# Optimization experiments

Measured on AMD Instinct MI355X. Metric: run time of the kernel, lower is better.

## Reference

```python
import jax, jax.numpy as jnp
import numpy as np

NUM_HEADS = 8
HEAD_DIM = 64
D_MODEL = NUM_HEADS * HEAD_DIM  # 512
B, T = 4, 2048


def setup_inputs() -> dict:
    key = jax.random.key(0)
    k1, k2 = jax.random.split(key)
    x = jax.random.normal(k1, (B, T, D_MODEL), dtype=jnp.float32)
    mask = jnp.ones((B, 1, T, T), dtype=jnp.float32)
    W = jax.random.normal(k2, (D_MODEL, 3 * D_MODEL), dtype=jnp.float32) * (D_MODEL ** -0.5)
    b = jnp.zeros((3 * D_MODEL,), dtype=jnp.float32)
    return {"x": x, "mask": mask, "W": W, "b": b}


def reference(x, mask, W, b):
    batch = x.shape[0]
    # fused QKV projection: [B, T, 3D]
    qkv = jnp.einsum("btd,de->bte", x, W) + b
    # NOTE: faithful to torch reshape [B, T, H, Hd, 3] -> the size-3 axis is innermost
    qkv = qkv.reshape(batch, -1, NUM_HEADS, HEAD_DIM, 3)
    qkv = jnp.transpose(qkv, (4, 0, 2, 1, 3))  # [3, B, H, T, Hd]
    q, k, v = qkv[0], qkv[1], qkv[2]
    logits = jnp.einsum("bhqd,bhkd->bhqk", q, k) / (HEAD_DIM ** 0.5)
    logits = logits + (1.0 - mask) * -10000.0
    w = jax.nn.softmax(logits, axis=-1)
    out = jnp.einsum("bhqk,bhkd->bhqd", w, v)  # [B, H, T, Hd]
    out = jnp.transpose(out, (0, 2, 1, 3)).reshape(batch, -1, NUM_HEADS * HEAD_DIM)
    return out
```

## Files before the change

kernel.cpp:

```cpp
#include <hip/hip_runtime.h>
#include <hip/hip_bf16.h>
#include <stdint.h>

#define B_   4
#define T_   2048
#define H_   8
#define HD_  64
#define DM_  512
#define N3_  1536

typedef short bf_el;
typedef __attribute__((ext_vector_type(8))) bf_el bfrag;
typedef __attribute__((ext_vector_type(4))) bf_el bhalf4;
typedef __attribute__((ext_vector_type(4))) float ffrag;

#define SCALE_L2E  0.18033688011112043f
#define MASK_L2E   14426.950408889634f

static __device__ __forceinline__ unsigned short f2bf(float f) {
    union { float f; unsigned int i; } v; v.f = f;
    unsigned int r = v.i + 0x7fff + ((v.i >> 16) & 1);
    return (unsigned short)(r >> 16);
}
static __device__ __forceinline__ unsigned short f2bf_fast(float f) {
    union { float f; unsigned int i; } v; v.f = f;
    return (unsigned short)((v.i + 0x8000u) >> 16);
}

static __device__ __forceinline__ unsigned int cvt_pk_bf16(float a, float b) {
    unsigned int r;
    asm("v_cvt_pk_bf16_f32 %0, %1, %2" : "=v"(r) : "v"(a), "v"(b));
    return r;
}

typedef __attribute__((address_space(1))) const unsigned int gu32;
typedef __attribute__((address_space(3))) unsigned int lu32;
static __device__ __forceinline__ void glds16(const unsigned short* g, unsigned short* l) {
    __builtin_amdgcn_global_load_lds((gu32*)g, (lu32*)l, 16, 0, 0);
}

#define VMCNT(n) do { asm volatile("s_waitcnt vmcnt(" #n ")" ::: "memory"); \
                      __builtin_amdgcn_sched_barrier(0); } while (0)

__global__ __launch_bounds__(256) void k_prep(const float* __restrict__ W,
                                              const float* __restrict__ X,
                                              const float* __restrict__ mask,
                                              unsigned short* __restrict__ Wt,
                                              unsigned short* __restrict__ Xb,
                                              int* __restrict__ flags) {
    __shared__ __align__(16) unsigned short Ls[64 * 72];
    const int bid = blockIdx.x;
    const int tid = threadIdx.x;

    if (bid < 512) {
        const int R0 = bid * 16;
        const int mb = R0 >> 11;
        const int q0 = R0 & 2047;
        const int e  = mb * 32 + (q0 >> 6);
        const int wave = tid >> 6, lane = tid & 63;
        unsigned int acc = 0u;
        const float* base = mask + (size_t)R0 * T_ + tid * 8;
#pragma unroll
        for (int rr = 0; rr < 16; ++rr) {
            const uint4 u0 = *(const uint4*)(base + (size_t)rr * T_);
            const uint4 u1 = *(const uint4*)(base + (size_t)rr * T_ + 4);
            acc |= (u0.x ^ 0x3F800000u) | (u0.y ^ 0x3F800000u) |
                   (u0.z ^ 0x3F800000u) | (u0.w ^ 0x3F800000u) |
                   (u1.x ^ 0x3F800000u) | (u1.y ^ 0x3F800000u) |
                   (u1.z ^ 0x3F800000u) | (u1.w ^ 0x3F800000u);
        }
        unsigned long long bal = __ballot(acc != 0u);
        if (lane == 0 && bal != 0ULL) {
            unsigned int bits = 0u;
#pragma unroll
            for (int j = 0; j < 8; ++j)
                if ((bal >> (8 * j)) & 0xFFULL)
                    bits |= (1u << (wave * 8 + j));
            atomicOr((unsigned int*)&flags[e], bits);
        }
        return;
    }
    if (bid < 768) {
        const int b2 = bid - 512;
        const float* src = X + (size_t)b2 * 16384;
        unsigned short* dst = Xb + (size_t)b2 * 16384;
#pragma unroll
        for (int j = 0; j < 8; ++j) {
            int idx = j * 512 + tid * 2;
            float4 f0 = *(const float4*)(src + idx * 4);
            float4 f1 = *(const float4*)(src + idx * 4 + 4);
            __align__(16) unsigned short t8[8];
            t8[0] = f2bf_fast(f0.x); t8[1] = f2bf_fast(f0.y);
            t8[2] = f2bf_fast(f0.z); t8[3] = f2bf_fast(f0.w);
            t8[4] = f2bf_fast(f1.x); t8[5] = f2bf_fast(f1.y);
            t8[6] = f2bf_fast(f1.z); t8[7] = f2bf_fast(f1.w);
            *(uint4*)(dst + idx * 4) = *(const uint4*)t8;
        }
        return;
    }
    {
        const int t  = bid - 768;
        const int n0 = (t % 24) * 64;
        const int k0 = (t / 24) * 64;
#pragma unroll
        for (int i = 0; i < 4; ++i) {
            int chunk = tid + i * 256;
            int k = chunk >> 4;
            int c = chunk & 15;
            float4 f = *(const float4*)(W + (size_t)(k0 + k) * N3_ + n0 + c * 4);
            unsigned short* p = Ls + k * 72 + c * 4;
            p[0] = f2bf(f.x); p[1] = f2bf(f.y); p[2] = f2bf(f.z); p[3] = f2bf(f.w);
        }
        __syncthreads();
        const int n = tid >> 2;
        const int g = tid & 3;
        __align__(16) unsigned short tmp[16];
#pragma unroll
        for (int i = 0; i < 16; ++i) tmp[i] = Ls[(g * 16 + i) * 72 + n];
        uint4* dst = (uint4*)(Wt + (size_t)(n0 + n) * DM_ + k0 + g * 16);
        dst[0] = *(const uint4*)(tmp);
        dst[1] = *(const uint4*)(tmp + 8);
    }
}

__global__ __launch_bounds__(256) void k_gemm_qkv(const unsigned short* __restrict__ Xb,
                                                  const unsigned short* __restrict__ Wt,
                                                  const float* __restrict__ bias,
                                                  unsigned short* __restrict__ Qb,
                                                  unsigned short* __restrict__ Kb,
                                                  unsigned short* __restrict__ Vtb) {
    __shared__ __align__(16) unsigned short SH[12800];
    unsigned short* As = SH;
    unsigned short* Bs = SH + 5120;
    unsigned short* Cs = SH;

    const int tid  = threadIdx.x;
    const int wave = tid >> 6;
    const int lane = tid & 63;
    const int quad = lane >> 4;
    const int l16  = lane & 15;
    const int wm = wave >> 1, wn = wave & 1;
    const int h  = blockIdx.x >> 6;
    const int m0 = (blockIdx.x & 63) * 128;
    const int n0 = h * 192;

    float bvv[6];
#pragma unroll
    for (int ni = 0; ni < 6; ++ni) bvv[ni] = bias[n0 + wn * 96 + ni * 16 + l16];

    ffrag acc[4][6];
#pragma unroll
    for (int i = 0; i < 4; ++i)
#pragma unroll
        for (int j = 0; j < 6; ++j) acc[i][j] = (ffrag){0.f, 0.f, 0.f, 0.f};

    for (int kt = 0; kt < 16; ++kt) {
        __syncthreads();
#pragma unroll
        for (int i = 0; i < 2; ++i) {
            int chunk = tid + i * 256;
            int r = chunk >> 2, c = chunk & 3;
            *(uint4*)(As + r * 40 + c * 8) =
                *(const uint4*)(Xb + (size_t)(m0 + r) * DM_ + kt * 32 + c * 8);
        }
#pragma unroll
        for (int i = 0; i < 3; ++i) {
            int chunk = tid + i * 256;
            int r = chunk >> 2, c = chunk & 3;
            *(uint4*)(Bs + r * 40 + c * 8) =
                *(const uint4*)(Wt + (size_t)(n0 + r) * DM_ + kt * 32 + c * 8);
        }
        __syncthreads();
        bfrag af[4], bfr[6];
#pragma unroll
        for (int mi = 0; mi < 4; ++mi)
            af[mi] = *(const bfrag*)(As + (wm * 64 + mi * 16 + l16) * 40 + quad * 8);
#pragma unroll
        for (int ni = 0; ni < 6; ++ni)
            bfr[ni] = *(const bfrag*)(Bs + (wn * 96 + ni * 16 + l16) * 40 + quad * 8);
#pragma unroll
        for (int mi = 0; mi < 4; ++mi)
#pragma unroll
            for (int ni = 0; ni < 6; ++ni)
                acc[mi][ni] = __builtin_amdgcn_mfma_f32_16x16x32_bf16(af[mi], bfr[ni], acc[mi][ni], 0, 0, 0);
    }

    const int b   = m0 >> 11;
    const int tb0 = m0 & 2047;
    const size_t bh = (size_t)(b * 8 + h);
    float cscale[6];
#pragma unroll
    for (int ni = 0; ni < 6; ++ni) {
        int c = wn * 96 + ni * 16 + l16;
        cscale[ni] = (c % 3 == 0) ? SCALE_L2E : 1.0f;
    }
#pragma unroll
    for (int half = 0; half < 2; ++half) {
        __syncthreads();
        if (wm == half) {
#pragma unroll
            for (int mi = 0; mi < 4; ++mi)
#pragma unroll
                for (int ni = 0; ni < 6; ++ni)
#pragma unroll
                    for (int reg = 0; reg < 4; ++reg) {
                        int r = mi * 16 + quad * 4 + reg;
                        int c = wn * 96 + ni * 16 + l16;
                        Cs[r * 200 + c] = f2bf_fast((acc[mi][ni][reg] + bvv[ni]) * cscale[ni]);
                    }
        }
        __syncthreads();
        const int tb = tb0 + half * 64;
#pragma unroll
        for (int i = 0; i < 2; ++i) {
            int idx = tid + i * 256;
            int tl = idx >> 3, hc = (idx & 7) * 8;
            __align__(16) unsigned short tq[8], tk[8];
#pragma unroll
            for (int j = 0; j < 8; ++j) {
                tq[j] = Cs[tl * 200 + (hc + j) * 3 + 0];
                tk[j] = Cs[tl * 200 + (hc + j) * 3 + 1];
            }
            *(uint4*)(Qb + (bh * T_ + tb + tl) * HD_ + hc) = *(const uint4*)tq;
            *(uint4*)(Kb + (bh * T_ + tb + tl) * HD_ + hc) = *(const uint4*)tk;
        }
#pragma unroll
        for (int i = 0; i < 2; ++i) {
            int idx = tid + i * 256;
            int hd = idx >> 3, t8 = (idx & 7) * 8;
            __align__(16) unsigned short tv[8];
#pragma unroll
            for (int j = 0; j < 8; ++j)
                tv[j] = Cs[(t8 + j) * 200 + hd * 3 + 2];
            *(uint4*)(Vtb + (bh * HD_ + hd) * T_ + tb + t8) = *(const uint4*)tv;
        }
    }
}

__global__ __launch_bounds__(256, 2) void k_attn(const unsigned short* __restrict__ Q,
                                                 const unsigned short* __restrict__ K,
                                                 const unsigned short* __restrict__ Vt,
                                                 const float* __restrict__ mask,
                                                 const int* __restrict__ flags,
                                                 float* __restrict__ out) {
    __shared__ __align__(16) unsigned short SH[32768];
    __shared__ float Rs[256];

    const int tid = threadIdx.x;
    const int wave = tid >> 6, lane = tid & 63;
    const int quad = lane >> 4, l16 = lane & 15;
    const int rg = wave & 1;
    const int kh = wave >> 1;
    const int bh = blockIdx.x & 31, b = bh >> 3, h = bh & 7;
    const int qt = blockIdx.x >> 5;
    const int q0 = qt * 128;

    bfrag qf[4][2];
#pragma unroll
    for (int g = 0; g < 4; ++g) {
        size_t qrow = ((size_t)bh * T_ + q0 + rg * 64 + g * 16 + l16) * HD_;
        qf[g][0] = *(const bfrag*)(Q + qrow + quad * 8);
        qf[g][1] = *(const bfrag*)(Q + qrow + 32 + quad * 8);
    }
    ffrag of[4][5];
#pragma unroll
    for (int g = 0; g < 4; ++g)
#pragma unroll
        for (int nb = 0; nb < 5; ++nb) of[g][nb] = (ffrag){0.f, 0.f, 0.f, 0.f};

    bfrag vones;
#pragma unroll
    for (int j = 0; j < 8; ++j) vones[j] = (short)0x3F80;

    const unsigned int flbits = ((const unsigned int*)flags)[b * 32 + qt * 2 + rg];

    const int lrow = lane >> 3, lcol = lane & 7, swz = lcol ^ lrow;
    const int voffK = lrow * 64 + swz * 8;
    const size_t voffV = (size_t)(wave * 16 + lrow) * T_ + swz * 8;
    const unsigned short* Kbh = K  + (size_t)bh * T_ * HD_;
    const unsigned short* Vbh = Vt + (size_t)bh * HD_ * T_;

    auto STAGE = [&](int buf, int kt) {
        unsigned short* KL = &SH[buf * 4096] + wave * 1024;
        unsigned short* VL = &SH[16384 + buf * 4096] + wave * 1024;
        const unsigned short* kg = Kbh + (size_t)kt * 4096 + wave * 1024 + voffK;
        const unsigned short* vg = Vbh + (size_t)kt * 64 + voffV;
        glds16(kg, KL);
        glds16(kg + 512, KL + 512);
        glds16(vg, VL);
        glds16(vg + (size_t)8 * T_, VL + 512);
    };

    STAGE(0, 0);
    STAGE(1, 1);

    for (int kt = 0; kt < 32; ++kt) {
        if (kt < 30) STAGE((kt + 2) & 3, kt + 2);
        if (kt < 30)      { VMCNT(8); }
        else if (kt == 30){ VMCNT(4); }
        else              { VMCNT(0); }
        __builtin_amdgcn_s_barrier();

        const int cur = kt & 3;
        const unsigned short* KLc = &SH[cur * 4096];
        const unsigned short* VLc = &SH[16384 + cur * 4096];

        bfrag kf[2][2];
#pragma unroll
        for (int ns = 0; ns < 2; ++ns) {
            const int r = (kh * 2 + ns) * 16 + l16;
#pragma unroll
            for (int ks = 0; ks < 2; ++ks)
                kf[ns][ks] = *(const bfrag*)(KLc + r * 64 + (((ks * 4 + quad) ^ (l16 & 7)) * 8));
        }
        bhalf4 vf[2][4];
#pragma unroll
        for (int nb = 0; nb < 4; ++nb) {
            const int d = nb * 16 + l16;
#pragma unroll
            for (int ns = 0; ns < 2; ++ns)
                vf[ns][nb] = *(const bhalf4*)(VLc + d * 64 +
                                ((kh * 32 + ns * 16 + quad * 4) ^ ((l16 & 7) * 8)));
        }

        const int fl = (int)((flbits >> kt) & 1u);
#pragma unroll
        for (int g = 0; g < 4; ++g) {
            ffrag st[2];
            __builtin_amdgcn_s_setprio(1);
#pragma unroll
            for (int ns = 0; ns < 2; ++ns) {
                ffrag a = (ffrag){0.f, 0.f, 0.f, 0.f};
                a = __builtin_amdgcn_mfma_f32_16x16x32_bf16(kf[ns][0], qf[g][0], a, 0, 0, 0);
                a = __builtin_amdgcn_mfma_f32_16x16x32_bf16(kf[ns][1], qf[g][1], a, 0, 0, 0);
                st[ns] = a;
            }
            __builtin_amdgcn_s_setprio(0);
            float p[2][4];
            if (fl) {
                const float* mrow = mask + ((size_t)b * T_ + q0 + rg * 64 + g * 16 + l16) * T_
                                  + kt * 64 + kh * 32 + quad * 4;
#pragma unroll
                for (int ns = 0; ns < 2; ++ns) {
                    float mv[4];
                    *(float4*)mv = *(const float4*)(mrow + ns * 16);
#pragma unroll
                    for (int reg = 0; reg < 4; ++reg)
                        p[ns][reg] = __builtin_amdgcn_exp2f(
                            fmaf(mv[reg], MASK_L2E, st[ns][reg] - MASK_L2E));
                }
            } else {
#pragma unroll
                for (int ns = 0; ns < 2; ++ns)
#pragma unroll
                    for (int reg = 0; reg < 4; ++reg)
                        p[ns][reg] = __builtin_amdgcn_exp2f(st[ns][reg]);
            }
            union { unsigned int u[4]; bfrag s; } pa;
            pa.u[0] = cvt_pk_bf16(p[0][0], p[0][1]);
            pa.u[1] = cvt_pk_bf16(p[0][2], p[0][3]);
            pa.u[2] = cvt_pk_bf16(p[1][0], p[1][1]);
            pa.u[3] = cvt_pk_bf16(p[1][2], p[1][3]);
            __builtin_amdgcn_s_setprio(1);
#pragma unroll
            for (int nb = 0; nb < 4; ++nb) {
                union { bhalf4 h[2]; bfrag f; } vv;
                vv.h[0] = vf[0][nb];
                vv.h[1] = vf[1][nb];
                of[g][nb] = __builtin_amdgcn_mfma_f32_16x16x32_bf16(pa.s, vv.f, of[g][nb], 0, 0, 0);
            }
            of[g][4] = __builtin_amdgcn_mfma_f32_16x16x32_bf16(pa.s, vones, of[g][4], 0, 0, 0);
            __builtin_amdgcn_s_setprio(0);
        }
    }

    __syncthreads();
    float* Fp = (float*)SH;
    if (l16 == 0) {
#pragma unroll
        for (int g = 0; g < 4; ++g)
#pragma unroll
            for (int reg = 0; reg < 4; ++reg)
                Rs[kh * 128 + rg * 64 + g * 16 + quad * 4 + reg] = of[g][4][reg];
    }
    if (kh == 1) {
        float* basep = Fp + rg * (64 * 66);
#pragma unroll
        for (int g = 0; g < 4; ++g)
#pragma unroll
            for (int nb = 0; nb < 4; ++nb)
#pragma unroll
                for (int reg = 0; reg < 4; ++reg)
                    basep[(g * 16 + quad * 4 + reg) * 66 + nb * 16 + l16] = of[g][nb][reg];
    }
    __syncthreads();
    if (kh == 0) {
        const float* basep = Fp + rg * (64 * 66);
#pragma unroll
        for (int g = 0; g < 4; ++g) {
            float inv[4];
#pragma unroll
            for (int reg = 0; reg < 4; ++reg) {
                int row = rg * 64 + g * 16 + quad * 4 + reg;
                inv[reg] = 1.0f / (Rs[row] + Rs[128 + row]);
            }
#pragma unroll
            for (int nb = 0; nb < 4; ++nb)
#pragma unroll
                for (int reg = 0; reg < 4; ++reg) {
                    float v = of[g][nb][reg] + basep[(g * 16 + quad * 4 + reg) * 66 + nb * 16 + l16];
                    int t = q0 + rg * 64 + g * 16 + quad * 4 + reg;
                    out[((size_t)b * T_ + t) * DM_ + h * 64 + nb * 16 + l16] = v * inv[reg];
                }
        }
    }
}

extern "C" void kernel_launch(void* const* d_in, const int* in_sizes, int n_in,
                              void* d_out, int out_size, void* d_ws, size_t ws_size,
                              hipStream_t stream) {
    const float* X    = (const float*)d_in[0];
    const float* mask = (const float*)d_in[1];
    const float* W    = (const float*)d_in[2];
    const float* bias = (const float*)d_in[3];
    float* outp = (float*)d_out;

    char* ws = (char*)d_ws;
    unsigned short* Wt  = (unsigned short*)(ws);
    unsigned short* Xb  = (unsigned short*)(ws + 1572864);
    unsigned short* Qb  = (unsigned short*)(ws + 9961472);
    unsigned short* Kb  = (unsigned short*)(ws + 18350080);
    unsigned short* Vtb = (unsigned short*)(ws + 26738688);
    int*            flg = (int*)(ws + 35127296);

    hipMemsetAsync(flg, 0, 512, stream);
    k_prep     <<<dim3(960), 256, 0, stream>>>(W, X, mask, Wt, Xb, flg);
    k_gemm_qkv <<<dim3(512), 256, 0, stream>>>(Xb, Wt, bias, Qb, Kb, Vtb);
    k_attn     <<<dim3(512), 256, 0, stream>>>(Qb, Kb, Vtb, mask, flg, outp);
}
```

Before: 196.3 us.

## Double-buffer QKV GEMM tiles and replace flag memset/atomics with per-block byte writes

The QKV GEMM now prefetches the next K-slice into registers while MFMAs run on the current shared-memory buffer, then writes it to a second LDS buffer. This leaves one barrier per iteration instead of two and overlaps global loads with compute. The mask-flag scan now has each wave store a byte into a dedicated slot instead of doing an atomicOr, so the hipMemsetAsync before the kernels can be dropped. The attention kernel ORs four words to rebuild the flags. Doubling LDS may reduce occupancy, and the flag buffer now grows to 2KB, which must fit inside the workspace.

```diff
diff --git a/kernel.cpp b/kernel.cpp
--- a/kernel.cpp
+++ b/kernel.cpp
@@ -70,13 +70,13 @@
                    (u1.z ^ 0x3F800000u) | (u1.w ^ 0x3F800000u);
         }
         unsigned long long bal = __ballot(acc != 0u);
-        if (lane == 0 && bal != 0ULL) {
-            unsigned int bits = 0u;
+        if (lane == 0) {
+            unsigned int byte = 0u;
 #pragma unroll
             for (int j = 0; j < 8; ++j)
-                if ((bal >> (8 * j)) & 0xFFULL)
-                    bits |= (1u << (wave * 8 + j));
-            atomicOr((unsigned int*)&flags[e], bits);
+                if ((bal >> (8 * j)) & 0xFFULL) byte |= (1u << j);
+            ((unsigned char*)flags)[((size_t)e * 4 + (bid & 3)) * 4 + wave] =
+                (unsigned char)byte;
         }
         return;
     }
@@ -129,9 +129,7 @@
                                                   unsigned short* __restrict__ Qb,
                                                   unsigned short* __restrict__ Kb,
                                                   unsigned short* __restrict__ Vtb) {
-    __shared__ __align__(16) unsigned short SH[12800];
-    unsigned short* As = SH;
-    unsigned short* Bs = SH + 5120;
+    __shared__ __align__(16) unsigned short SH[25600];
     unsigned short* Cs = SH;
 
     const int tid  = threadIdx.x;
@@ -154,23 +152,46 @@
 #pragma unroll
         for (int j = 0; j < 6; ++j) acc[i][j] = (ffrag){0.f, 0.f, 0.f, 0.f};
 
-    for (int kt = 0; kt < 16; ++kt) {
-        __syncthreads();
+    uint4 areg[2], breg[3];
+    auto GLOAD = [&](int kt) {
 #pragma unroll
         for (int i = 0; i < 2; ++i) {
             int chunk = tid + i * 256;
             int r = chunk >> 2, c = chunk & 3;
-            *(uint4*)(As + r * 40 + c * 8) =
-                *(const uint4*)(Xb + (size_t)(m0 + r) * DM_ + kt * 32 + c * 8);
+            areg[i] = *(const uint4*)(Xb + (size_t)(m0 + r) * DM_ + kt * 32 + c * 8);
         }
 #pragma unroll
         for (int i = 0; i < 3; ++i) {
             int chunk = tid + i * 256;
             int r = chunk >> 2, c = chunk & 3;
-            *(uint4*)(Bs + r * 40 + c * 8) =
-                *(const uint4*)(Wt + (size_t)(n0 + r) * DM_ + kt * 32 + c * 8);
-        }
-        __syncthreads();
+            breg[i] = *(const uint4*)(Wt + (size_t)(n0 + r) * DM_ + kt * 32 + c * 8);
+        }
+    };
+    auto SWRITE = [&](int buf) {
+        unsigned short* As = SH + buf * 12800;
+        unsigned short* Bs = As + 5120;
+#pragma unroll
+        for (int i = 0; i < 2; ++i) {
+            int chunk = tid + i * 256;
+            int r = chunk >> 2, c = chunk & 3;
+            *(uint4*)(As + r * 40 + c * 8) = areg[i];
+        }
+#pragma unroll
+        for (int i = 0; i < 3; ++i) {
+            int chunk = tid + i * 256;
+            int r = chunk >> 2, c = chunk & 3;
+            *(uint4*)(Bs + r * 40 + c * 8) = breg[i];
+        }
+    };
+
+    GLOAD(0); SWRITE(0);
+    __syncthreads();
+
+    for (int kt = 0; kt < 16; ++kt) {
+        const int cur = kt & 1;
+        if (kt < 15) GLOAD(kt + 1);
+        const unsigned short* As = SH + cur * 12800;
+        const unsigned short* Bs = As + 5120;
         bfrag af[4], bfr[6];
 #pragma unroll
         for (int mi = 0; mi < 4; ++mi)
@@ -183,6 +204,10 @@
 #pragma unroll
             for (int ni = 0; ni < 6; ++ni)
                 acc[mi][ni] = __builtin_amdgcn_mfma_f32_16x16x32_bf16(af[mi], bfr[ni], acc[mi][ni], 0, 0, 0);
+        if (kt < 15) {
+            SWRITE(cur ^ 1);
+            __syncthreads();
+        }
     }
 
     const int b   = m0 >> 11;
@@ -272,7 +297,9 @@
 #pragma unroll
     for (int j = 0; j < 8; ++j) vones[j] = (short)0x3F80;
 
-    const unsigned int flbits = ((const unsigned int*)flags)[b * 32 + qt * 2 + rg];
+    const int e = b * 32 + qt * 2 + rg;
+    const int4 fw = *(const int4*)(flags + (size_t)e * 4);
+    const unsigned int flbits = (unsigned int)(fw.x | fw.y | fw.z | fw.w);
 
     const int lrow = lane >> 3, lcol = lane & 7, swz = lcol ^ lrow;
     const int voffK = lrow * 64 + swz * 8;
@@ -433,7 +460,6 @@
     unsigned short* Vtb = (unsigned short*)(ws + 26738688);
     int*            flg = (int*)(ws + 35127296);
 
-    hipMemsetAsync(flg, 0, 512, stream);
     k_prep     <<<dim3(960), 256, 0, stream>>>(W, X, mask, Wt, Xb, flg);
     k_gemm_qkv <<<dim3(512), 256, 0, stream>>>(Xb, Wt, bias, Qb, Kb, Vtb);
     k_attn     <<<dim3(512), 256, 0, stream>>>(Qb, Kb, Vtb, mask, flg, outp);
```

New measurement: 221.3 us. 12.7% more time.

## Pipeline QKV GEMM loads via async global-to-LDS and drop flag memset

Applied to the files above, without the earlier changes.

The QKV GEMM now stages A and B tiles straight into LDS with async global-to-LDS loads, using a 4-deep ring buffer with two tiles in flight. Progress is tracked with vmcnt waits and a single barrier, and the LDS layout is XOR-swizzled, which removes the register round-trip and one of the two syncthreads per k-step. The mask-flag pass now writes a plain byte per wave into an expanded flag array that attention ORs back together, so the memset launch and the atomics go away. The cost is much more LDS per block (80 KB), which may limit occupancy. The flag buffer grows 4x, so the workspace layout must still fit.

```diff
diff --git a/kernel.cpp b/kernel.cpp
--- a/kernel.cpp
+++ b/kernel.cpp
@@ -70,13 +70,13 @@
                    (u1.z ^ 0x3F800000u) | (u1.w ^ 0x3F800000u);
         }
         unsigned long long bal = __ballot(acc != 0u);
-        if (lane == 0 && bal != 0ULL) {
-            unsigned int bits = 0u;
+        if (lane == 0) {
+            unsigned int byte = 0u;
 #pragma unroll
             for (int j = 0; j < 8; ++j)
-                if ((bal >> (8 * j)) & 0xFFULL)
-                    bits |= (1u << (wave * 8 + j));
-            atomicOr((unsigned int*)&flags[e], bits);
+                if ((bal >> (8 * j)) & 0xFFULL) byte |= (1u << j);
+            ((unsigned char*)flags)[((size_t)e * 4 + (bid & 3)) * 4 + wave] =
+                (unsigned char)byte;
         }
         return;
     }
@@ -129,9 +129,7 @@
                                                   unsigned short* __restrict__ Qb,
                                                   unsigned short* __restrict__ Kb,
                                                   unsigned short* __restrict__ Vtb) {
-    __shared__ __align__(16) unsigned short SH[12800];
-    unsigned short* As = SH;
-    unsigned short* Bs = SH + 5120;
+    __shared__ __align__(16) unsigned short SH[40960];
     unsigned short* Cs = SH;
 
     const int tid  = threadIdx.x;
@@ -154,35 +152,50 @@
 #pragma unroll
         for (int j = 0; j < 6; ++j) acc[i][j] = (ffrag){0.f, 0.f, 0.f, 0.f};
 
+    const int lrow = lane >> 2;
+    const int gslot = (lane & 3) ^ (lrow & 3);
+    const unsigned short* Ag = Xb + (size_t)(m0 + wave * 32 + lrow) * DM_ + gslot * 8;
+    const unsigned short* Bg = Wt + (size_t)(n0 + wave * 48 + lrow) * DM_ + gslot * 8;
+
+    auto STAGE = [&](int buf, int kt) {
+        unsigned short* AL = SH + buf * 10240 + wave * 1024;
+        unsigned short* BL = SH + buf * 10240 + 4096 + wave * 1536;
+        const unsigned short* ag = Ag + kt * 32;
+        const unsigned short* bg = Bg + kt * 32;
+        glds16(ag, AL);
+        glds16(ag + (size_t)16 * DM_, AL + 512);
+        glds16(bg, BL);
+        glds16(bg + (size_t)16 * DM_, BL + 512);
+        glds16(bg + (size_t)32 * DM_, BL + 1024);
+    };
+
+    STAGE(0, 0);
+    STAGE(1, 1);
+
     for (int kt = 0; kt < 16; ++kt) {
-        __syncthreads();
-#pragma unroll
-        for (int i = 0; i < 2; ++i) {
-            int chunk = tid + i * 256;
-            int r = chunk >> 2, c = chunk & 3;
-            *(uint4*)(As + r * 40 + c * 8) =
-                *(const uint4*)(Xb + (size_t)(m0 + r) * DM_ + kt * 32 + c * 8);
-        }
-#pragma unroll
-        for (int i = 0; i < 3; ++i) {
-            int chunk = tid + i * 256;
-            int r = chunk >> 2, c = chunk & 3;
-            *(uint4*)(Bs + r * 40 + c * 8) =
-                *(const uint4*)(Wt + (size_t)(n0 + r) * DM_ + kt * 32 + c * 8);
-        }
-        __syncthreads();
+        if (kt < 14) STAGE((kt + 2) & 3, kt + 2);
+        if (kt < 14)      { VMCNT(10); }
+        else if (kt == 14){ VMCNT(5); }
+        else              { VMCNT(0); }
+        __builtin_amdgcn_s_barrier();
+
+        const unsigned short* As = SH + (kt & 3) * 10240;
+        const unsigned short* Bs = As + 4096;
+        const int rslot = (quad ^ (l16 & 3)) * 8;
         bfrag af[4], bfr[6];
 #pragma unroll
         for (int mi = 0; mi < 4; ++mi)
-            af[mi] = *(const bfrag*)(As + (wm * 64 + mi * 16 + l16) * 40 + quad * 8);
+            af[mi] = *(const bfrag*)(As + (wm * 64 + mi * 16 + l16) * 32 + rslot);
 #pragma unroll
         for (int ni = 0; ni < 6; ++ni)
-            bfr[ni] = *(const bfrag*)(Bs + (wn * 96 + ni * 16 + l16) * 40 + quad * 8);
+            bfr[ni] = *(const bfrag*)(Bs + (wn * 96 + ni * 16 + l16) * 32 + rslot);
+        __builtin_amdgcn_s_setprio(1);
 #pragma unroll
         for (int mi = 0; mi < 4; ++mi)
 #pragma unroll
             for (int ni = 0; ni < 6; ++ni)
                 acc[mi][ni] = __builtin_amdgcn_mfma_f32_16x16x32_bf16(af[mi], bfr[ni], acc[mi][ni], 0, 0, 0);
+        __builtin_amdgcn_s_setprio(0);
     }
 
     const int b   = m0 >> 11;
@@ -272,7 +285,9 @@
 #pragma unroll
     for (int j = 0; j < 8; ++j) vones[j] = (short)0x3F80;
 
-    const unsigned int flbits = ((const unsigned int*)flags)[b * 32 + qt * 2 + rg];
+    const int e = b * 32 + qt * 2 + rg;
+    const int4 fw = *(const int4*)(flags + (size_t)e * 4);
+    const unsigned int flbits = (unsigned int)(fw.x | fw.y | fw.z | fw.w);
 
     const int lrow = lane >> 3, lcol = lane & 7, swz = lcol ^ lrow;
     const int voffK = lrow * 64 + swz * 8;
@@ -433,7 +448,6 @@
     unsigned short* Vtb = (unsigned short*)(ws + 26738688);
     int*            flg = (int*)(ws + 35127296);
 
-    hipMemsetAsync(flg, 0, 512, stream);
     k_prep     <<<dim3(960), 256, 0, stream>>>(W, X, mask, Wt, Xb, flg);
     k_gemm_qkv <<<dim3(512), 256, 0, stream>>>(Xb, Wt, bias, Qb, Kb, Vtb);
     k_attn     <<<dim3(512), 256, 0, stream>>>(Qb, Kb, Vtb, mask, flg, outp);
```

Result: faster. 183.5 us (median of 2 runs) (-6.5%).
